# Kernel optimization log

Hardware: AMD Instinct MI355X
Metric: run time of the kernel (lower is better)

The kernel has to match this reference:

```python
import jax, jax.numpy as jnp
import numpy as np

N, C_IN, C_OUT, P, W, H = 32, 32, 16, 4, 16, 16
D = P * P
EPS = 1e-6


def squash(s, axis=-1):
    # v = ||s||^2/(1+||s||^2) * s/||s||, eps-stabilized as in the repo (eps=1e-6)
    n2 = jnp.sum(s * s, axis=axis, keepdims=True)
    n = jnp.sqrt(n2)
    return (n2 / (1.0 + n2)) * s / (n + EPS)


def setup_inputs() -> dict:
    key = jax.random.key(0)
    k1, k2, k3 = jax.random.split(key, 3)
    l = jax.random.normal(k1, (N, C_IN, D, W, H), jnp.float32)
    g = jax.random.normal(k2, (N, C_OUT, D), jnp.float32)
    weight = jax.random.normal(k3, (1, C_IN, 1, C_OUT, P, P), jnp.float32)
    return {"l": l, "g": g, "weight": weight, "num_iters": 3}


def reference(l, g, weight, num_iters):
    n, c, d, w, h = l.shape
    p = weight.shape[-1]
    c_out = weight.shape[3]
    # (N, C, D, W, H) -> (N, C, W*H, P, P)
    lp = jnp.transpose(l, (0, 1, 3, 4, 2)).reshape(n, c, w * h, p, p)
    # votes: pose matmul against per-(in,out) transform matrices
    # v[n,c,s,o] = lp[n,c,s] @ weight[0,c,0,o]   -> (N, C, WH, C_out, P, P)
    v = jnp.einsum('ncsij,cojk->ncsoik', lp, weight[0, :, 0])
    M = c * w * h
    v = v.reshape(n, M, c_out, d)          # (N, M, C_out, D)
    g = g[:, None, :, :]                    # (N, 1, C_out, D)
    # dynamic routing, logits initialized from agreement with the prior global capsule g
    b = jnp.sum(v * g, axis=-1, keepdims=True)   # (N, M, C_out, 1)
    cc = None
    for _ in range(num_iters):
        cc = jax.nn.softmax(b, axis=1)           # attention over input votes M
        g = squash(jnp.sum(cc * v, axis=1, keepdims=True))  # (N, 1, C_out, D)
        b = b + jnp.sum(v * g, axis=-1, keepdims=True)
    a = jnp.squeeze(cc, -1)   # (N, M, C_out)
    g = jnp.squeeze(g, 1)     # (N, C_out, D)
    return a, g
```

## Files before the change

### kernel.cpp

```cpp
#include <hip/hip_runtime.h>
#include <math.h>

#define N_   32
#define CIN  32
#define COUT 16
#define D_   16
#define S_   256
#define M_   (CIN * S_)

#define LOG2E 1.4426950408889634f

#define PROW 20
#define PIDX(n, c, o) ((((size_t)(n) * CIN + (c)) * COUT + (o)) * PROW)

#define WS_PB0 0
#define WS_PB1 (N_ * CIN * COUT * PROW)
#define WS_G1  (2 * N_ * CIN * COUT * PROW)

#define SW(s) ((((s) & 3)) ^ (((s) >> 2) & 3))

__device__ __forceinline__ void stage_load(const float* __restrict__ gsrc,
                                           int tid, float4* vals) {
  const float4* src = (const float4*)gsrc;
#pragma unroll
  for (int j = 0; j < 4; j++)
    vals[j] = src[((tid & 3) << 6) + (tid >> 2) + (j << 8)];
}

__device__ __forceinline__ void stage_store(float* ls, int tid,
                                            const float4* vals) {
#pragma unroll
  for (int j = 0; j < 4; j++) {
    int f = ((tid & 3) << 6) + (tid >> 2) + (j << 8);
    int dd = f >> 6;
    int u  = f & 63;
    int chunk = dd >> 2, lo = dd & 3;
    float vv[4] = {vals[j].x, vals[j].y, vals[j].z, vals[j].w};
#pragma unroll
    for (int m = 0; m < 4; m++) {
      int s = (u << 2) + m;
      int p = chunk ^ SW(s);
      ls[(s << 4) + (p << 2) + lo] = vv[m];
    }
  }
}

__device__ __forceinline__ void read_lp(const float* ls, int s, float* lp) {
  const float4* row = (const float4*)(ls + (s << 4));
  int sw = SW(s);
#pragma unroll
  for (int c = 0; c < 4; c++) {
    float4 q = row[c ^ sw];
    lp[c * 4 + 0] = q.x; lp[c * 4 + 1] = q.y;
    lp[c * 4 + 2] = q.z; lp[c * 4 + 3] = q.w;
  }
}

__device__ __forceinline__ float dot16(const float* a, const float* b) {
  float a0 = 0.f, a1 = 0.f, a2 = 0.f, a3 = 0.f;
#pragma unroll
  for (int k = 0; k < 4; k++) {
    a0 = fmaf(a[k],      b[k],      a0);
    a1 = fmaf(a[4 + k],  b[4 + k],  a1);
    a2 = fmaf(a[8 + k],  b[8 + k],  a2);
    a3 = fmaf(a[12 + k], b[12 + k], a3);
  }
  return (a0 + a1) + (a2 + a3);
}

__device__ __forceinline__ void make_WG(const float* __restrict__ wgt,
                                        int c, int o, const float* Greg,
                                        float* WG) {
  float wreg[16];
  const float4* wp = (const float4*)(wgt + (c * COUT + o) * 16);
#pragma unroll
  for (int i = 0; i < 4; i++) {
    float4 t = wp[i];
    wreg[i * 4 + 0] = t.x; wreg[i * 4 + 1] = t.y;
    wreg[i * 4 + 2] = t.z; wreg[i * 4 + 3] = t.w;
  }
#pragma unroll
  for (int i = 0; i < 4; i++)
#pragma unroll
    for (int j = 0; j < 4; j++) {
      float acc = 0.f;
#pragma unroll
      for (int k = 0; k < 4; k++)
        acc = fmaf(wreg[j * 4 + k], Greg[i * 4 + k], acc);
      WG[i * 4 + j] = acc * LOG2E;
    }
}

__device__ __forceinline__ void sweep(const float* ls, const float* WG,
                                      float shift, int strip, int doDump,
                                      float* __restrict__ edp,
                                      float& se, float& bmx, float* E) {
  se = 0.f; bmx = -INFINITY;
#pragma unroll
  for (int d = 0; d < 16; d++) E[d] = 0.f;
#pragma unroll 4
  for (int it = 0; it < 16; it++) {
    float lp[16];
    read_lp(ls, strip + (it << 4), lp);
    float b = dot16(lp, WG) - shift;
    float e = exp2f(b);
    if (doDump) edp[(size_t)(it << 4) * COUT] = e;
    bmx = fmaxf(bmx, b);
    se += e;
#pragma unroll
    for (int d = 0; d < 16; d++) E[d] = fmaf(e, lp[d], E[d]);
  }
#pragma unroll
  for (int off = 16; off <= 32; off <<= 1) {
    se += __shfl_xor(se, off);
    bmx = fmaxf(bmx, __shfl_xor(bmx, off));
#pragma unroll
    for (int d = 0; d < 16; d++) E[d] += __shfl_xor(E[d], off);
  }
}

__device__ __forceinline__ void tail_store(const float* __restrict__ wgt,
                                           int c, int o,
                                           float (*red2)[16],
                                           float* __restrict__ part_out,
                                           int n, float shift) {
  float wt[16];
  const float4* wp = (const float4*)(wgt + (c * COUT + o) * 16);
#pragma unroll
  for (int i = 0; i < 4; i++) {
    float4 t = wp[i];
    wt[i * 4 + 0] = t.x; wt[i * 4 + 1] = t.y;
    wt[i * 4 + 2] = t.z; wt[i * 4 + 3] = t.w;
  }
  float Et[16];
#pragma unroll
  for (int d = 0; d < 16; d++) Et[d] = red2[d][o];
  float* p0 = part_out + PIDX(n, c, o);
  float4* p4 = (float4*)p0;
#pragma unroll
  for (int i = 0; i < 4; i++) {
    float s0 = 0.f, s1 = 0.f, s2 = 0.f, s3 = 0.f;
#pragma unroll
    for (int j = 0; j < 4; j++) {
      s0 = fmaf(Et[i * 4 + j], wt[j * 4 + 0], s0);
      s1 = fmaf(Et[i * 4 + j], wt[j * 4 + 1], s1);
      s2 = fmaf(Et[i * 4 + j], wt[j * 4 + 2], s2);
      s3 = fmaf(Et[i * 4 + j], wt[j * 4 + 3], s3);
    }
    p4[i] = make_float4(s0, s1, s2, s3);
  }
  p0[16] = red2[16][o];
  p0[17] = red2[17][o] + shift;
}

#define MERGE_STORE(w_, o_, E_, se_, bmx_)           \
  do {                                               \
    if ((tid & 63) < 16) {                           \
      _Pragma("unroll")                              \
      for (int d = 0; d < 16; d++) red[w_][d][o_] = E_[d]; \
      red[w_][16][o_] = se_;                         \
      red[w_][17][o_] = bmx_;                        \
    }                                                \
  } while (0)

__global__ __launch_bounds__(256, 3) void pass_kernel(
    const float* __restrict__ l, const float* __restrict__ wgt,
    const float* __restrict__ gprev, const float* __restrict__ part_in,
    float* __restrict__ gstore, float* __restrict__ part_out,
    float* __restrict__ edump, int mode) {
  const int bid = blockIdx.x;
  const int n  = bid >> 4;
  const int c0 = bid & 15;
  const int c1 = c0 + 16;
  const int tid = threadIdx.x;
  const int o = tid & 15;
  const int strip = tid >> 4;
  const int w = tid >> 6;

  __shared__ float ls[D_ * S_];
  __shared__ float red[4][18][16];
  __shared__ float red2[18][16];
  __shared__ float hd[16][20];

  if (mode && tid < 64) {
    const int ho = tid & 15, hs = tid >> 4;
    float H[18];
#pragma unroll
    for (int f = 0; f < 17; f++) H[f] = 0.f;
    H[17] = -INFINITY;
#pragma unroll 2
    for (int q = 0; q < 8; q++) {
      const float* r = part_in + PIDX(n, hs + 4 * q, ho);
      const float4* r4 = (const float4*)r;
#pragma unroll
      for (int i = 0; i < 4; i++) {
        float4 v = r4[i];
        H[i * 4 + 0] += v.x; H[i * 4 + 1] += v.y;
        H[i * 4 + 2] += v.z; H[i * 4 + 3] += v.w;
      }
      H[16] += r[16];
      H[17] = fmaxf(H[17], r[17]);
    }
#pragma unroll
    for (int off = 16; off <= 32; off <<= 1) {
#pragma unroll
      for (int f = 0; f < 17; f++) H[f] += __shfl_xor(H[f], off);
      H[17] = fmaxf(H[17], __shfl_xor(H[17], off));
    }
    if (tid < 16) {
      float inv = 1.0f / H[16], n2 = 0.f, Sg[16];
#pragma unroll
      for (int d = 0; d < 16; d++) { Sg[d] = H[d] * inv; n2 = fmaf(Sg[d], Sg[d], n2); }
      float coef = n2 / ((1.f + n2) * (sqrtf(n2) + 1e-6f));
      float4* hq = (float4*)hd[tid];
#pragma unroll
      for (int i = 0; i < 4; i++)
        hq[i] = make_float4(coef * Sg[i * 4 + 0], coef * Sg[i * 4 + 1],
                            coef * Sg[i * 4 + 2], coef * Sg[i * 4 + 3]);
      hd[tid][16] = H[17];
    }
  }

  {
    float4 va[4];
    stage_load(l + ((size_t)(n * CIN + c0)) * D_ * S_, tid, va);
    stage_store(ls, tid, va);
  }

  float Greg[16];
  {
    const float4* gp = (const float4*)(gprev + (n * COUT + o) * 16);
#pragma unroll
    for (int i = 0; i < 4; i++) {
      float4 u = gp[i];
      Greg[i * 4 + 0] = u.x; Greg[i * 4 + 1] = u.y;
      Greg[i * 4 + 2] = u.z; Greg[i * 4 + 3] = u.w;
    }
  }

  __syncthreads();

  float shift = 0.f;
  if (mode) {
    const float4* hq = (const float4*)hd[o];
#pragma unroll
    for (int i = 0; i < 4; i++) {
      float4 v = hq[i];
      Greg[i * 4 + 0] += v.x; Greg[i * 4 + 1] += v.y;
      Greg[i * 4 + 2] += v.z; Greg[i * 4 + 3] += v.w;
    }
    shift = hd[o][16];
    if (mode == 1 && c0 == 0 && tid < 16) {
      const float4* hp = (const float4*)hd[tid];
      const float4* gp = (const float4*)(gprev + (n * COUT + tid) * 16);
      float4* g4 = (float4*)(gstore + (n * COUT + tid) * 16);
#pragma unroll
      for (int i = 0; i < 4; i++) {
        float4 a = gp[i], b = hp[i];
        g4[i] = make_float4(a.x + b.x, a.y + b.y, a.z + b.z, a.w + b.w);
      }
    }
  }

  float4 vb[4];
  stage_load(l + ((size_t)(n * CIN + c1)) * D_ * S_, tid, vb);

  float WG[16];
  make_WG(wgt, c0, o, Greg, WG);
  float se, bmx, E[16];
  {
    float* edp = edump
        ? edump + ((size_t)(n * M_ + c0 * S_ + strip)) * COUT + o : nullptr;
    sweep(ls, WG, shift, strip, edump != nullptr, edp, se, bmx, E);
  }

  MERGE_STORE(w, o, E, se, bmx);
  __syncthreads();

  stage_store(ls, tid, vb);

  for (int p = tid; p < 288; p += 256) {
    int f = p >> 4, oo = p & 15;
    float v0 = red[0][f][oo], v1 = red[1][f][oo];
    float v2 = red[2][f][oo], v3 = red[3][f][oo];
    red2[f][oo] = (f == 17) ? fmaxf(fmaxf(v0, v1), fmaxf(v2, v3))
                            : ((v0 + v1) + (v2 + v3));
  }
  __syncthreads();

  if (tid < 16) tail_store(wgt, c0, tid, red2, part_out, n, shift);

  make_WG(wgt, c1, o, Greg, WG);
  {
    float* edp = edump
        ? edump + ((size_t)(n * M_ + c1 * S_ + strip)) * COUT + o : nullptr;
    sweep(ls, WG, shift, strip, edump != nullptr, edp, se, bmx, E);
  }

  MERGE_STORE(w, o, E, se, bmx);
  __syncthreads();

  for (int p = tid; p < 288; p += 256) {
    int f = p >> 4, oo = p & 15;
    float v0 = red[0][f][oo], v1 = red[1][f][oo];
    float v2 = red[2][f][oo], v3 = red[3][f][oo];
    red2[f][oo] = (f == 17) ? fmaxf(fmaxf(v0, v1), fmaxf(v2, v3))
                            : ((v0 + v1) + (v2 + v3));
  }
  __syncthreads();

  if (tid < 16) tail_store(wgt, c1, tid, red2, part_out, n, shift);
}

__global__ __launch_bounds__(256, 4) void a_kernel(
    const float* __restrict__ part, float* __restrict__ a_out,
    float* __restrict__ g_out) {
  const int bid = blockIdx.x;
  const int n = bid >> 5;
  const int chunk = bid & 31;
  const int tid = threadIdx.x;

  __shared__ float sinv[16];

  if (tid < 16) {
    float se = 0.f;
    if (chunk == 0) {
      float S[16];
#pragma unroll
      for (int d = 0; d < 16; d++) S[d] = 0.f;
#pragma unroll 4
      for (int c = 0; c < CIN; c++) {
        const float* r = part + PIDX(n, c, tid);
        const float4* r4 = (const float4*)r;
#pragma unroll
        for (int i = 0; i < 4; i++) {
          float4 v = r4[i];
          S[i * 4 + 0] += v.x; S[i * 4 + 1] += v.y;
          S[i * 4 + 2] += v.z; S[i * 4 + 3] += v.w;
        }
        se += r[16];
      }
      float inv = 1.0f / se, n2 = 0.f;
#pragma unroll
      for (int d = 0; d < 16; d++) { S[d] *= inv; n2 = fmaf(S[d], S[d], n2); }
      float coef = n2 / ((1.f + n2) * (sqrtf(n2) + 1e-6f));
      float* go = g_out + (n * COUT + tid) * 16;
#pragma unroll
      for (int d = 0; d < 16; d++) go[d] = coef * S[d];
      sinv[tid] = inv;
    } else {
#pragma unroll 8
      for (int c = 0; c < CIN; c++) se += part[PIDX(n, c, tid) + 16];
      sinv[tid] = 1.0f / se;
    }
  }
  __syncthreads();

  float4* pv = (float4*)(a_out + (size_t)n * (M_ * COUT) + (size_t)chunk * 4096);
#pragma unroll
  for (int r = 0; r < 4; r++) {
    int i4 = tid + (r << 8);
    int o0 = (i4 & 3) << 2;
    float4 v = pv[i4];
    v.x *= sinv[o0 + 0];
    v.y *= sinv[o0 + 1];
    v.z *= sinv[o0 + 2];
    v.w *= sinv[o0 + 3];
    pv[i4] = v;
  }
}

extern "C" void kernel_launch(void* const* d_in, const int* in_sizes, int n_in,
                              void* d_out, int out_size, void* d_ws, size_t ws_size,
                              hipStream_t stream) {
  const float* l = (const float*)d_in[0];
  const float* g = (const float*)d_in[1];
  const float* w = (const float*)d_in[2];

  float* out = (float*)d_out;
  float* ws = (float*)d_ws;
  float* a_out = out;
  float* g_out = out + (size_t)N_ * M_ * COUT;

  float* PB0 = ws + WS_PB0;
  float* PB1 = ws + WS_PB1;
  float* G1  = ws + WS_G1;

  pass_kernel<<<N_ * 16, 256, 0, stream>>>(l, w, g, nullptr, nullptr, PB0,
                                           nullptr, 0);
  pass_kernel<<<N_ * 16, 256, 0, stream>>>(l, w, g, PB0, G1, PB1,
                                           nullptr, 1);
  pass_kernel<<<N_ * 16, 256, 0, stream>>>(l, w, G1, PB1, nullptr, PB0,
                                           a_out, 2);
  a_kernel<<<N_ * 32, 256, 0, stream>>>(PB0, a_out, g_out);
}
```

Measured before the change: 120.8 us.

## Fuse three routing passes and normalization into one persistent kernel with grid barriers

Replaces the three pass launches and the a_kernel normalization with a single persistent kernel. Each block keeps both input-capsule tiles resident in shared memory (two 16 KB buffers) across all iterations, so l is read from HBM once instead of three times. Iterations are separated by a software grid barrier built on atomic counters in the workspace, which is zeroed with a memset. The barrier requires all 512 blocks to be co-resident. Raising shared memory per block and lowering launch bounds to 2 blocks per CU make that occupancy requirement tighter and risk deadlock or spin overhead.

```diff
diff --git a/kernel.cpp b/kernel.cpp
--- a/kernel.cpp
+++ b/kernel.cpp
@@ -13,9 +13,8 @@
 #define PROW 20
 #define PIDX(n, c, o) ((((size_t)(n) * CIN + (c)) * COUT + (o)) * PROW)
 
-#define WS_PB0 0
-#define WS_PB1 (N_ * CIN * COUT * PROW)
-#define WS_G1  (2 * N_ * CIN * COUT * PROW)
+#define WS_PB0 1024
+#define WS_PB1 (WS_PB0 + N_ * CIN * COUT * PROW)
 
 #define SW(s) ((((s) & 3)) ^ (((s) >> 2) & 3))
 
@@ -120,8 +119,7 @@
 }
 
 __device__ __forceinline__ void tail_store(const float* __restrict__ wgt,
-                                           int c, int o,
-                                           float (*red2)[16],
+                                           int c, int o, float (*red2)[16],
                                            float* __restrict__ part_out,
                                            int n, float shift) {
   float wt[16];
@@ -153,36 +151,41 @@
   p0[17] = red2[17][o] + shift;
 }
 
-#define MERGE_STORE(w_, o_, E_, se_, bmx_)           \
-  do {                                               \
-    if ((tid & 63) < 16) {                           \
-      _Pragma("unroll")                              \
-      for (int d = 0; d < 16; d++) red[w_][d][o_] = E_[d]; \
-      red[w_][16][o_] = se_;                         \
-      red[w_][17][o_] = bmx_;                        \
-    }                                                \
-  } while (0)
-
-__global__ __launch_bounds__(256, 3) void pass_kernel(
-    const float* __restrict__ l, const float* __restrict__ wgt,
-    const float* __restrict__ gprev, const float* __restrict__ part_in,
-    float* __restrict__ gstore, float* __restrict__ part_out,
-    float* __restrict__ edump, int mode) {
-  const int bid = blockIdx.x;
-  const int n  = bid >> 4;
-  const int c0 = bid & 15;
-  const int c1 = c0 + 16;
-  const int tid = threadIdx.x;
-  const int o = tid & 15;
-  const int strip = tid >> 4;
-  const int w = tid >> 6;
-
-  __shared__ float ls[D_ * S_];
-  __shared__ float red[4][18][16];
-  __shared__ float red2[18][16];
-  __shared__ float hd[16][20];
-
-  if (mode && tid < 64) {
+__device__ __forceinline__ void pass_tile(const float* ls,
+                                          const float* __restrict__ wgt,
+                                          int c, int n, const float* Greg,
+                                          float shift, float* edump,
+                                          float* part_out,
+                                          float (*red)[18][16],
+                                          float (*red2)[16], int tid) {
+  const int o = tid & 15, strip = tid >> 4, w = tid >> 6;
+  float WG[16];
+  make_WG(wgt, c, o, Greg, WG);
+  float se, bmx, E[16];
+  float* edp = edump
+      ? edump + ((size_t)(n * M_ + c * S_ + strip)) * COUT + o : nullptr;
+  sweep(ls, WG, shift, strip, edump != nullptr, edp, se, bmx, E);
+  if ((tid & 63) < 16) {
+#pragma unroll
+    for (int d = 0; d < 16; d++) red[w][d][o] = E[d];
+    red[w][16][o] = se;
+    red[w][17][o] = bmx;
+  }
+  __syncthreads();
+  for (int p = tid; p < 288; p += 256) {
+    int f = p >> 4, oo = p & 15;
+    float v0 = red[0][f][oo], v1 = red[1][f][oo];
+    float v2 = red[2][f][oo], v3 = red[3][f][oo];
+    red2[f][oo] = (f == 17) ? fmaxf(fmaxf(v0, v1), fmaxf(v2, v3))
+                            : ((v0 + v1) + (v2 + v3));
+  }
+  __syncthreads();
+  if (tid < 16) tail_store(wgt, c, tid, red2, part_out, n, shift);
+}
+
+__device__ __forceinline__ void head_hd(const float* __restrict__ part,
+                                        int n, int tid, float (*hd)[20]) {
+  if (tid < 64) {
     const int ho = tid & 15, hs = tid >> 4;
     float H[18];
 #pragma unroll
@@ -190,7 +193,7 @@
     H[17] = -INFINITY;
 #pragma unroll 2
     for (int q = 0; q < 8; q++) {
-      const float* r = part_in + PIDX(n, hs + 4 * q, ho);
+      const float* r = part + PIDX(n, hs + 4 * q, ho);
       const float4* r4 = (const float4*)r;
 #pragma unroll
       for (int i = 0; i < 4; i++) {
@@ -218,18 +221,68 @@
         hq[i] = make_float4(coef * Sg[i * 4 + 0], coef * Sg[i * 4 + 1],
                             coef * Sg[i * 4 + 2], coef * Sg[i * 4 + 3]);
       hd[tid][16] = H[17];
-    }
-  }
+      hd[tid][17] = inv;
+    }
+  }
+}
+
+__device__ __forceinline__ unsigned agent_load(unsigned* p) {
+#if __has_builtin(__hip_atomic_load)
+  return __hip_atomic_load(p, __ATOMIC_RELAXED, __HIP_MEMORY_SCOPE_AGENT);
+#else
+  return atomicAdd(p, 0u);
+#endif
+}
+
+__device__ __forceinline__ void grid_barrier(unsigned* bar, int n, int phase,
+                                             int tid) {
+  __syncthreads();
+  if (tid == 0) {
+    __threadfence();
+    unsigned prev = atomicAdd(&bar[n * 16], 1u);
+    if (prev + 1 == (unsigned)(phase * 16)) atomicAdd(&bar[512], 1u);
+    while (agent_load(&bar[512]) < (unsigned)(phase * 32))
+      __builtin_amdgcn_s_sleep(32);
+    __threadfence();
+  }
+  __syncthreads();
+}
+
+__global__ __launch_bounds__(256, 2) void fused_kernel(
+    const float* __restrict__ l, const float* __restrict__ wgt,
+    const float* __restrict__ g0, float* __restrict__ ws_f,
+    unsigned* __restrict__ bar, float* __restrict__ a_out,
+    float* __restrict__ g_out) {
+  const int bid = blockIdx.x;
+  const int n  = bid >> 4;
+  const int c0 = bid & 15;
+  const int c1 = c0 + 16;
+  const int tid = threadIdx.x;
+  const int o = tid & 15;
+
+  __shared__ float lsA[D_ * S_];
+  __shared__ float lsB[D_ * S_];
+  __shared__ float red[4][18][16];
+  __shared__ float red2[18][16];
+  __shared__ float hd[16][20];
+
+  float* PB0 = ws_f + WS_PB0;
+  float* PB1 = ws_f + WS_PB1;
 
   {
     float4 va[4];
     stage_load(l + ((size_t)(n * CIN + c0)) * D_ * S_, tid, va);
-    stage_store(ls, tid, va);
+    stage_store(lsA, tid, va);
+  }
+  {
+    float4 vb[4];
+    stage_load(l + ((size_t)(n * CIN + c1)) * D_ * S_, tid, vb);
+    stage_store(lsB, tid, vb);
   }
 
   float Greg[16];
   {
-    const float4* gp = (const float4*)(gprev + (n * COUT + o) * 16);
+    const float4* gp = (const float4*)(g0 + (n * COUT + o) * 16);
 #pragma unroll
     for (int i = 0; i < 4; i++) {
       float4 u = gp[i];
@@ -241,7 +294,14 @@
   __syncthreads();
 
   float shift = 0.f;
-  if (mode) {
+
+  pass_tile(lsA, wgt, c0, n, Greg, shift, nullptr, PB0, red, red2, tid);
+  pass_tile(lsB, wgt, c1, n, Greg, shift, nullptr, PB0, red, red2, tid);
+  grid_barrier(bar, n, 1, tid);
+
+  head_hd(PB0, n, tid, hd);
+  __syncthreads();
+  {
     const float4* hq = (const float4*)hd[o];
 #pragma unroll
     for (int i = 0; i < 4; i++) {
@@ -250,123 +310,51 @@
       Greg[i * 4 + 2] += v.z; Greg[i * 4 + 3] += v.w;
     }
     shift = hd[o][16];
-    if (mode == 1 && c0 == 0 && tid < 16) {
-      const float4* hp = (const float4*)hd[tid];
-      const float4* gp = (const float4*)(gprev + (n * COUT + tid) * 16);
-      float4* g4 = (float4*)(gstore + (n * COUT + tid) * 16);
-#pragma unroll
-      for (int i = 0; i < 4; i++) {
-        float4 a = gp[i], b = hp[i];
-        g4[i] = make_float4(a.x + b.x, a.y + b.y, a.z + b.z, a.w + b.w);
-      }
-    }
-  }
-
-  float4 vb[4];
-  stage_load(l + ((size_t)(n * CIN + c1)) * D_ * S_, tid, vb);
-
-  float WG[16];
-  make_WG(wgt, c0, o, Greg, WG);
-  float se, bmx, E[16];
-  {
-    float* edp = edump
-        ? edump + ((size_t)(n * M_ + c0 * S_ + strip)) * COUT + o : nullptr;
-    sweep(ls, WG, shift, strip, edump != nullptr, edp, se, bmx, E);
-  }
-
-  MERGE_STORE(w, o, E, se, bmx);
-  __syncthreads();
-
-  stage_store(ls, tid, vb);
-
-  for (int p = tid; p < 288; p += 256) {
-    int f = p >> 4, oo = p & 15;
-    float v0 = red[0][f][oo], v1 = red[1][f][oo];
-    float v2 = red[2][f][oo], v3 = red[3][f][oo];
-    red2[f][oo] = (f == 17) ? fmaxf(fmaxf(v0, v1), fmaxf(v2, v3))
-                            : ((v0 + v1) + (v2 + v3));
-  }
-  __syncthreads();
-
-  if (tid < 16) tail_store(wgt, c0, tid, red2, part_out, n, shift);
-
-  make_WG(wgt, c1, o, Greg, WG);
-  {
-    float* edp = edump
-        ? edump + ((size_t)(n * M_ + c1 * S_ + strip)) * COUT + o : nullptr;
-    sweep(ls, WG, shift, strip, edump != nullptr, edp, se, bmx, E);
-  }
-
-  MERGE_STORE(w, o, E, se, bmx);
-  __syncthreads();
-
-  for (int p = tid; p < 288; p += 256) {
-    int f = p >> 4, oo = p & 15;
-    float v0 = red[0][f][oo], v1 = red[1][f][oo];
-    float v2 = red[2][f][oo], v3 = red[3][f][oo];
-    red2[f][oo] = (f == 17) ? fmaxf(fmaxf(v0, v1), fmaxf(v2, v3))
-                            : ((v0 + v1) + (v2 + v3));
-  }
-  __syncthreads();
-
-  if (tid < 16) tail_store(wgt, c1, tid, red2, part_out, n, shift);
-}
-
-__global__ __launch_bounds__(256, 4) void a_kernel(
-    const float* __restrict__ part, float* __restrict__ a_out,
-    float* __restrict__ g_out) {
-  const int bid = blockIdx.x;
-  const int n = bid >> 5;
-  const int chunk = bid & 31;
-  const int tid = threadIdx.x;
-
-  __shared__ float sinv[16];
-
-  if (tid < 16) {
-    float se = 0.f;
-    if (chunk == 0) {
-      float S[16];
-#pragma unroll
-      for (int d = 0; d < 16; d++) S[d] = 0.f;
-#pragma unroll 4
-      for (int c = 0; c < CIN; c++) {
-        const float* r = part + PIDX(n, c, tid);
-        const float4* r4 = (const float4*)r;
-#pragma unroll
-        for (int i = 0; i < 4; i++) {
-          float4 v = r4[i];
-          S[i * 4 + 0] += v.x; S[i * 4 + 1] += v.y;
-          S[i * 4 + 2] += v.z; S[i * 4 + 3] += v.w;
-        }
-        se += r[16];
-      }
-      float inv = 1.0f / se, n2 = 0.f;
-#pragma unroll
-      for (int d = 0; d < 16; d++) { S[d] *= inv; n2 = fmaf(S[d], S[d], n2); }
-      float coef = n2 / ((1.f + n2) * (sqrtf(n2) + 1e-6f));
-      float* go = g_out + (n * COUT + tid) * 16;
-#pragma unroll
-      for (int d = 0; d < 16; d++) go[d] = coef * S[d];
-      sinv[tid] = inv;
-    } else {
-#pragma unroll 8
-      for (int c = 0; c < CIN; c++) se += part[PIDX(n, c, tid) + 16];
-      sinv[tid] = 1.0f / se;
-    }
-  }
-  __syncthreads();
-
-  float4* pv = (float4*)(a_out + (size_t)n * (M_ * COUT) + (size_t)chunk * 4096);
-#pragma unroll
-  for (int r = 0; r < 4; r++) {
-    int i4 = tid + (r << 8);
-    int o0 = (i4 & 3) << 2;
-    float4 v = pv[i4];
-    v.x *= sinv[o0 + 0];
-    v.y *= sinv[o0 + 1];
-    v.z *= sinv[o0 + 2];
-    v.w *= sinv[o0 + 3];
-    pv[i4] = v;
+  }
+  pass_tile(lsA, wgt, c0, n, Greg, shift, nullptr, PB1, red, red2, tid);
+  pass_tile(lsB, wgt, c1, n, Greg, shift, nullptr, PB1, red, red2, tid);
+  grid_barrier(bar, n, 2, tid);
+
+  head_hd(PB1, n, tid, hd);
+  __syncthreads();
+  {
+    const float4* hq = (const float4*)hd[o];
+#pragma unroll
+    for (int i = 0; i < 4; i++) {
+      float4 v = hq[i];
+      Greg[i * 4 + 0] += v.x; Greg[i * 4 + 1] += v.y;
+      Greg[i * 4 + 2] += v.z; Greg[i * 4 + 3] += v.w;
+    }
+    shift = hd[o][16];
+  }
+  pass_tile(lsA, wgt, c0, n, Greg, shift, a_out, PB0, red, red2, tid);
+  pass_tile(lsB, wgt, c1, n, Greg, shift, a_out, PB0, red, red2, tid);
+  grid_barrier(bar, n, 3, tid);
+
+  head_hd(PB0, n, tid, hd);
+  __syncthreads();
+
+  if (c0 == 0 && tid < 16) {
+    const float4* hq = (const float4*)hd[tid];
+    float4* g4 = (float4*)(g_out + (n * COUT + tid) * 16);
+#pragma unroll
+    for (int i = 0; i < 4; i++) g4[i] = hq[i];
+  }
+
+  const int q = tid & 3;
+  float s0 = hd[(q << 2) + 0][17], s1 = hd[(q << 2) + 1][17];
+  float s2 = hd[(q << 2) + 2][17], s3 = hd[(q << 2) + 3][17];
+#pragma unroll
+  for (int t = 0; t < 2; t++) {
+    const int c = t ? c1 : c0;
+    float4* pv = (float4*)(a_out + ((size_t)(n * M_ + c * S_)) * COUT);
+#pragma unroll
+    for (int r = 0; r < 4; r++) {
+      int i4 = tid + (r << 8);
+      float4 v = pv[i4];
+      v.x *= s0; v.y *= s1; v.z *= s2; v.w *= s3;
+      pv[i4] = v;
+    }
   }
 }
 
@@ -382,15 +370,8 @@
   float* a_out = out;
   float* g_out = out + (size_t)N_ * M_ * COUT;
 
-  float* PB0 = ws + WS_PB0;
-  float* PB1 = ws + WS_PB1;
-  float* G1  = ws + WS_G1;
-
-  pass_kernel<<<N_ * 16, 256, 0, stream>>>(l, w, g, nullptr, nullptr, PB0,
-                                           nullptr, 0);
-  pass_kernel<<<N_ * 16, 256, 0, stream>>>(l, w, g, PB0, G1, PB1,
-                                           nullptr, 1);
-  pass_kernel<<<N_ * 16, 256, 0, stream>>>(l, w, G1, PB1, nullptr, PB0,
-                                           a_out, 2);
-  a_kernel<<<N_ * 32, 256, 0, stream>>>(PB0, a_out, g_out);
-}
+  hipMemsetAsync(d_ws, 0, 4096, stream);
+
+  fused_kernel<<<N_ * 16, 256, 0, stream>>>(l, w, g, ws, (unsigned*)d_ws,
+                                            a_out, g_out);
+}
```

New measurement: 198.9 us. 64.6% more time.
